# Kernel optimization log

Measured on AMD Instinct MI355X. Metric: run time of the kernel, lower is better.

## Reference

```python
import jax, jax.numpy as jnp
import numpy as np

N = 50000
E = 800000
EPS = 1e-5


def setup_inputs() -> dict:
    key = jax.random.key(0)
    ks = jax.random.split(key, 12)

    def w(k, fi, fo):
        return jax.random.normal(k, (fi, fo), dtype=jnp.float32) * (1.0 / np.sqrt(fi))

    return {
        "x": jax.random.normal(ks[0], (N, 128), dtype=jnp.float32),
        "edge_index": jax.random.randint(ks[1], (2, E), 0, N, dtype=jnp.int32),
        "W1": w(ks[2], 128, 256), "b1": jnp.zeros((256,), jnp.float32),
        "g1": jnp.ones((256,), jnp.float32), "be1": jnp.zeros((256,), jnp.float32),
        "W2": w(ks[3], 256, 128), "b2": jnp.zeros((128,), jnp.float32),
        "g2": jnp.ones((128,), jnp.float32), "be2": jnp.zeros((128,), jnp.float32),
        "W3": w(ks[4], 128, 64), "b3": jnp.zeros((64,), jnp.float32),
        "g3": jnp.ones((64,), jnp.float32), "be3": jnp.zeros((64,), jnp.float32),
        "W4": w(ks[5], 64, 40), "b4": jnp.zeros((40,), jnp.float32),
        "a": jnp.array(0.25, dtype=jnp.float32),  # PReLU single shared weight
    }


def _gcn_norm(edge_index, n):
    # PyG GCNConv default: add self-loops, symmetric normalization.
    loop = jnp.arange(n, dtype=edge_index.dtype)
    s = jnp.concatenate([edge_index[0], loop])  # [E+N] source nodes
    d = jnp.concatenate([edge_index[1], loop])  # [E+N] dest nodes
    deg = jax.ops.segment_sum(jnp.ones_like(s, dtype=jnp.float32), d, num_segments=n)
    dinv = jax.lax.rsqrt(jnp.maximum(deg, 1.0))  # deg >= 1 due to self-loops
    norm = dinv[s] * dinv[d]                     # [E+N]
    return s, d, norm


def _gcn_conv(x, W, b, s, d, norm, n):
    xw = x @ W                                   # [N, F_out] dense transform
    msg = xw[s] * norm[:, None]                  # gather + edge scaling
    return jax.ops.segment_sum(msg, d, num_segments=n) + b  # scatter-add


def _bn(x, g, b):
    # BatchNorm over nodes (training statistics, biased variance)
    m = jnp.mean(x, axis=0)
    v = jnp.var(x, axis=0)
    return (x - m) * jax.lax.rsqrt(v + EPS) * g + b


def _prelu(x, a):
    return jnp.where(x >= 0, x, a * x)


def reference(x, edge_index, W1, b1, g1, be1, W2, b2, g2, be2,
              W3, b3, g3, be3, W4, b4, a):
    n = x.shape[0]
    s, d, norm = _gcn_norm(edge_index, n)
    h = _prelu(_bn(_gcn_conv(x, W1, b1, s, d, norm, n), g1, be1), a)
    h = _prelu(_bn(_gcn_conv(h, W2, b2, s, d, norm, n), g2, be2), a)
    h = _prelu(_bn(_gcn_conv(h, W3, b3, s, d, norm, n), g3, be3), a)
    h = _gcn_conv(h, W4, b4, s, d, norm, n)
    return jax.nn.log_softmax(h, axis=1)
```

## Files before the change

### kernel.cpp

```cpp
#include <hip/hip_runtime.h>
#include <cstdint>
#include <cmath>

typedef _Float16 half_t;
typedef _Float16 h2 __attribute__((ext_vector_type(2)));
typedef _Float16 h8 __attribute__((ext_vector_type(8)));
typedef float f4 __attribute__((ext_vector_type(4)));


__global__ __launch_bounds__(256) void csr_hist_kernel(const int* __restrict__ ei_dst,
                                                       int* __restrict__ hcnt,
                                                       int E, int B, int NB, int chunk) {
    __shared__ int hist[256];
    int t = threadIdx.x;
    hist[t] = 0;
    __syncthreads();
    int base = blockIdx.x * chunk;
    int lim = min(base + chunk, E);
    for (int e = base + t; e < lim; e += 256) {
        int dst = ei_dst[e];
        atomicAdd(&hist[dst >> 8], 1);
    }
    __syncthreads();
    if (t < B) hcnt[t * NB + blockIdx.x] = hist[t];
}

__global__ __launch_bounds__(256) void csr_bscan_kernel(int* __restrict__ hcnt,
                                                        int* __restrict__ btot, int NB) {
    __shared__ int sh[256];
    int b = blockIdx.x, t = threadIdx.x;
    int v = (t < NB) ? hcnt[b * NB + t] : 0;
    sh[t] = v;
    __syncthreads();
    for (int off = 1; off < 256; off <<= 1) {
        int u = (t >= off) ? sh[t - off] : 0;
        __syncthreads();
        sh[t] += u;
        __syncthreads();
    }
    if (t < NB) hcnt[b * NB + t] = sh[t] - v;
    if (t == 255) btot[b] = sh[255];
}

__global__ __launch_bounds__(256) void csr_ebase_kernel(const int* __restrict__ btot,
                                                        int* __restrict__ edge_base,
                                                        int* __restrict__ row_ptr,
                                                        int B, int E, int n) {
    __shared__ int sh[256];
    int t = threadIdx.x;
    int v = (t < B) ? btot[t] : 0;
    sh[t] = v;
    __syncthreads();
    for (int off = 1; off < 256; off <<= 1) {
        int u = (t >= off) ? sh[t - off] : 0;
        __syncthreads();
        sh[t] += u;
        __syncthreads();
    }
    if (t < B) edge_base[t] = sh[t] - v;
    if (t == 0) {
        edge_base[B] = E;
        row_ptr[n] = E;
    }
}

__global__ __launch_bounds__(256) void csr_part_kernel(const int* __restrict__ ei,
                                                       const int* __restrict__ hcnt,
                                                       const int* __restrict__ edge_base,
                                                       unsigned int* __restrict__ ebuf,
                                                       int E, int B, int NB, int chunk) {
    __shared__ int lcur[256];
    int t = threadIdx.x;
    if (t < B) lcur[t] = edge_base[t] + hcnt[t * NB + blockIdx.x];
    __syncthreads();
    int base = blockIdx.x * chunk;
    int lim = min(base + chunk, E);
    for (int e = base + t; e < lim; e += 256) {
        int src = ei[e];
        int dst = ei[E + e];
        int b = dst >> 8;
        int pos = atomicAdd(&lcur[b], 1);
        ebuf[pos] = ((unsigned int)(dst & 255) << 16) | (unsigned int)src;
    }
}

__global__ __launch_bounds__(256) void csr_fill_kernel(const unsigned int* __restrict__ ebuf,
                                                       const int* __restrict__ edge_base,
                                                       int* __restrict__ row_ptr,
                                                       float* __restrict__ dinv,
                                                       unsigned short* __restrict__ colidx,
                                                       int n) {
    __shared__ int cnt[256];
    __shared__ int sc[256];
    __shared__ int cur[256];
    int b = blockIdx.x;
    int t = threadIdx.x;
    int seg_beg = edge_base[b];
    int seg_end = edge_base[b + 1];
    cnt[t] = 0;
    __syncthreads();
    for (int e = seg_beg + t; e < seg_end; e += 256)
        atomicAdd(&cnt[ebuf[e] >> 16], 1);
    __syncthreads();
    sc[t] = cnt[t];
    __syncthreads();
    for (int off = 1; off < 256; off <<= 1) {
        int u = (t >= off) ? sc[t - off] : 0;
        __syncthreads();
        sc[t] += u;
        __syncthreads();
    }
    int excl = seg_beg + sc[t] - cnt[t];
    int node = (b << 8) + t;
    if (node < n) {
        row_ptr[node] = excl;
        dinv[node] = rsqrtf((float)cnt[t] + 1.0f);
    }
    cur[t] = excl;
    __syncthreads();
    for (int e = seg_beg + t; e < seg_end; e += 256) {
        unsigned int p = ebuf[e];
        int pos = atomicAdd(&cur[p >> 16], 1);
        colidx[pos] = (unsigned short)(p & 0xffff);
    }
}


__global__ void f2h_kernel(const float* __restrict__ x, half_t* __restrict__ xh, int total4) {
    int i = blockIdx.x * blockDim.x + threadIdx.x;
    if (i < total4) {
        float4 v = *(const float4*)&x[i * 4];
        half_t* p = xh + (size_t)i * 4;
        p[0] = (half_t)v.x; p[1] = (half_t)v.y; p[2] = (half_t)v.z; p[3] = (half_t)v.w;
    }
}

__global__ void wt_kernel(const float* __restrict__ W, half_t* __restrict__ Wt,
                          int K, int Nc, int Ncp) {
    int idx = blockIdx.x * blockDim.x + threadIdx.x;
    if (idx >= Ncp * K) return;
    int n = idx / K, k = idx - n * K;
    Wt[idx] = (n < Nc) ? (half_t)W[(size_t)k * Nc + n] : (half_t)0.f;
}


__global__ __launch_bounds__(256) void aggh128_kernel(const half_t* __restrict__ in,
                                                      half_t* __restrict__ out,
                                                      const int* __restrict__ row_ptr,
                                                      const unsigned short* __restrict__ colidx,
                                                      const float* __restrict__ dinv, int n) {
    int node = blockIdx.x * 4 + (threadIdx.x >> 6);
    if (node >= n) return;
    int c = threadIdx.x & 63;
    float dv = dinv[node];
    h2 self = *(const h2*)(in + (size_t)node * 128 + 2 * c);
    float acc0 = dv * (float)self[0], acc1 = dv * (float)self[1];
    int beg = row_ptr[node], end = row_ptr[node + 1];
    int k = beg;
    for (; k + 3 < end; k += 4) {
        int s0 = colidx[k], s1 = colidx[k + 1], s2 = colidx[k + 2], s3 = colidx[k + 3];
        float d0 = dinv[s0], d1 = dinv[s1], d2 = dinv[s2], d3 = dinv[s3];
        h2 v0 = *(const h2*)(in + (size_t)s0 * 128 + 2 * c);
        h2 v1 = *(const h2*)(in + (size_t)s1 * 128 + 2 * c);
        h2 v2 = *(const h2*)(in + (size_t)s2 * 128 + 2 * c);
        h2 v3 = *(const h2*)(in + (size_t)s3 * 128 + 2 * c);
        acc0 = fmaf(d0, (float)v0[0], acc0); acc1 = fmaf(d0, (float)v0[1], acc1);
        acc0 = fmaf(d1, (float)v1[0], acc0); acc1 = fmaf(d1, (float)v1[1], acc1);
        acc0 = fmaf(d2, (float)v2[0], acc0); acc1 = fmaf(d2, (float)v2[1], acc1);
        acc0 = fmaf(d3, (float)v3[0], acc0); acc1 = fmaf(d3, (float)v3[1], acc1);
    }
    for (; k < end; ++k) {
        int s = colidx[k];
        float ds = dinv[s];
        h2 v = *(const h2*)(in + (size_t)s * 128 + 2 * c);
        acc0 = fmaf(ds, (float)v[0], acc0);
        acc1 = fmaf(ds, (float)v[1], acc1);
    }
    h2 r;
    r[0] = (half_t)(dv * acc0);
    r[1] = (half_t)(dv * acc1);
    *(h2*)(out + (size_t)node * 128 + 2 * c) = r;
}

__global__ __launch_bounds__(256) void aggh64_kernel(const half_t* __restrict__ in,
                                                     half_t* __restrict__ out,
                                                     const int* __restrict__ row_ptr,
                                                     const unsigned short* __restrict__ colidx,
                                                     const float* __restrict__ dinv, int n) {
    int node = blockIdx.x * 4 + (threadIdx.x >> 6);
    if (node >= n) return;
    int c = threadIdx.x & 63;
    float dv = dinv[node];
    float acc = dv * (float)in[(size_t)node * 64 + c];
    int beg = row_ptr[node], end = row_ptr[node + 1];
    int k = beg;
    for (; k + 3 < end; k += 4) {
        int s0 = colidx[k], s1 = colidx[k + 1], s2 = colidx[k + 2], s3 = colidx[k + 3];
        float d0 = dinv[s0], d1 = dinv[s1], d2 = dinv[s2], d3 = dinv[s3];
        float v0 = (float)in[(size_t)s0 * 64 + c];
        float v1 = (float)in[(size_t)s1 * 64 + c];
        float v2 = (float)in[(size_t)s2 * 64 + c];
        float v3 = (float)in[(size_t)s3 * 64 + c];
        acc = fmaf(d0, v0, acc);
        acc = fmaf(d1, v1, acc);
        acc = fmaf(d2, v2, acc);
        acc = fmaf(d3, v3, acc);
    }
    for (; k < end; ++k) {
        int s = colidx[k];
        acc = fmaf(dinv[s], (float)in[(size_t)s * 64 + c], acc);
    }
    out[(size_t)node * 64 + c] = (half_t)(dv * acc);
}

__global__ __launch_bounds__(256) void aggh_softmax_kernel(const half_t* __restrict__ in,
                                                           float* __restrict__ out,
                                                           const int* __restrict__ row_ptr,
                                                           const unsigned short* __restrict__ colidx,
                                                           const float* __restrict__ dinv,
                                                           const float* __restrict__ b4, int n) {
    int node = blockIdx.x * 4 + (threadIdx.x >> 6);
    if (node >= n) return;
    int c = threadIdx.x & 63;
    float dv = dinv[node];
    float acc = 0.f;
    if (c < 40) acc = dv * (float)in[(size_t)node * 40 + c];
    int beg = row_ptr[node], end = row_ptr[node + 1];
    int k = beg;
    for (; k + 3 < end; k += 4) {
        int s0 = colidx[k], s1 = colidx[k + 1], s2 = colidx[k + 2], s3 = colidx[k + 3];
        float d0 = dinv[s0], d1 = dinv[s1], d2 = dinv[s2], d3 = dinv[s3];
        if (c < 40) {
            float v0 = (float)in[(size_t)s0 * 40 + c];
            float v1 = (float)in[(size_t)s1 * 40 + c];
            float v2 = (float)in[(size_t)s2 * 40 + c];
            float v3 = (float)in[(size_t)s3 * 40 + c];
            acc = fmaf(d0, v0, acc);
            acc = fmaf(d1, v1, acc);
            acc = fmaf(d2, v2, acc);
            acc = fmaf(d3, v3, acc);
        }
    }
    for (; k < end; ++k) {
        int s = colidx[k];
        if (c < 40) acc = fmaf(dinv[s], (float)in[(size_t)s * 40 + c], acc);
    }
    float z = (c < 40) ? (dv * acc + b4[c]) : -INFINITY;
    float m = z;
#pragma unroll
    for (int off = 32; off > 0; off >>= 1) m = fmaxf(m, __shfl_xor(m, off, 64));
    float e = (c < 40) ? expf(z - m) : 0.f;
    float s = e;
#pragma unroll
    for (int off = 32; off > 0; off >>= 1) s += __shfl_xor(s, off, 64);
    if (c < 40) out[(size_t)node * 40 + c] = z - m - logf(s);
}


template <int K, int NT, bool FUSE>
__global__ __launch_bounds__(256) void mgemm_kernel(const half_t* __restrict__ A,
                                                    const half_t* __restrict__ Wt,
                                                    const float* __restrict__ AB,
                                                    const float* __restrict__ pa,
                                                    half_t* __restrict__ C,
                                                    int M, int Nc, int nTiles) {
    constexpr int NR = NT * 16;
    constexpr int CH = K / 8;
    constexpr int LOG_CH = (CH == 8) ? 3 : (CH == 16 ? 4 : 5);
    __shared__ half_t wlds[NR * K];

    for (int idx = threadIdx.x; idx < NR * CH; idx += 256) {
        int row = idx >> LOG_CH;
        int c = idx & (CH - 1);
        *(h8*)(wlds + ((size_t)c * NR + row) * 8) = *(const h8*)(Wt + (size_t)idx * 8);
    }
    int wave = threadIdx.x >> 6;
    int lane = threadIdx.x & 63;
    int l16 = lane & 15, kgrp = lane >> 4;
    float alpha = FUSE ? pa[0] : 0.f;
    __syncthreads();

    for (int tile = blockIdx.x; tile < nTiles; tile += gridDim.x) {
        int r0 = tile * 64 + wave * 16;
        int arow = r0 + l16;
        bool rowok = (arow < M);
        const half_t* Ap = A + (size_t)arow * K + kgrp * 8;
        h8 af[K / 32];
#pragma unroll
        for (int kk = 0; kk < K / 32; ++kk) {
            h8 v;
            if (rowok) {
                v = *(const h8*)(Ap + kk * 32);
            } else {
#pragma unroll
                for (int j = 0; j < 8; ++j) v[j] = (half_t)0.f;
            }
            if (FUSE) {
                int kb = kk * 32 + kgrp * 8;
#pragma unroll
                for (int j = 0; j < 8; ++j) {
                    float u = (float)v[j] * AB[kb + j] + AB[256 + kb + j];
                    u = (u >= 0.f) ? u : alpha * u;
                    v[j] = (half_t)u;
                }
            }
            af[kk] = v;
        }

        for (int nt = 0; nt < NT; ++nt) {
            f4 acc = {0.f, 0.f, 0.f, 0.f};
#pragma unroll
            for (int kk = 0; kk < K / 32; ++kk) {
                h8 bf = *(const h8*)(wlds + ((size_t)(kk * 4 + kgrp) * NR + nt * 16 + l16) * 8);
                acc = __builtin_amdgcn_mfma_f32_16x16x32_f16(af[kk], bf, acc, 0, 0, 0);
            }
            int col = nt * 16 + l16;
            if (col < Nc) {
#pragma unroll
                for (int j = 0; j < 4; ++j) {
                    int row = r0 + kgrp * 4 + j;
                    if (row < M) C[(size_t)row * Nc + col] = (half_t)acc[j];
                }
            }
        }
    }
}


template <int F>
__global__ __launch_bounds__(256) void stats2_kernel(const half_t* __restrict__ z,
                                                     float* __restrict__ sums, int n) {
    constexpr int CB = F / 8;
    constexpr int RG = 256 / CB;
    __shared__ float red[256][16];
    int t = threadIdx.x;
    int cb = t % CB;
    int rg = t / CB;
    float sm[8], sq[8];
#pragma unroll
    for (int j = 0; j < 8; ++j) { sm[j] = 0.f; sq[j] = 0.f; }
    for (int r = blockIdx.x * RG + rg; r < n; r += gridDim.x * RG) {
        h8 v = *(const h8*)(z + (size_t)r * F + cb * 8);
#pragma unroll
        for (int j = 0; j < 8; ++j) {
            float f = (float)v[j];
            sm[j] += f;
            sq[j] = fmaf(f, f, sq[j]);
        }
    }
#pragma unroll
    for (int j = 0; j < 8; ++j) { red[t][j] = sm[j]; red[t][8 + j] = sq[j]; }
    __syncthreads();
    for (int o = t; o < 2 * F; o += 256) {
        int c = o % F, kind = o / F;
        int cbo = c >> 3, ci = (c & 7) + kind * 8;
        float v = 0.f;
#pragma unroll
        for (int g = 0; g < RG; ++g) v += red[g * CB + cbo][ci];
        atomicAdd(&sums[kind * 256 + c], v);
    }
}

__global__ void bnfin_kernel(const float* __restrict__ sums, const float* __restrict__ g,
                             const float* __restrict__ be, float* __restrict__ AB, int n, int F) {
    int c = threadIdx.x;
    if (c >= F) return;
    float mean = sums[c] / (float)n;
    float var = sums[256 + c] / (float)n - mean * mean;
    float rstd = rsqrtf(var + 1e-5f);
    float sc = g[c] * rstd;
    AB[c] = sc;
    AB[256 + c] = be[c] - mean * sc;
}


extern "C" void kernel_launch(void* const* d_in, const int* in_sizes, int n_in,
                              void* d_out, int out_size, void* d_ws, size_t ws_size,
                              hipStream_t stream) {
    const float* x   = (const float*)d_in[0];
    const int*   ei  = (const int*)d_in[1];
    const float* W1  = (const float*)d_in[2];
    const float* g1  = (const float*)d_in[4];
    const float* be1 = (const float*)d_in[5];
    const float* W2  = (const float*)d_in[6];
    const float* g2  = (const float*)d_in[8];
    const float* be2 = (const float*)d_in[9];
    const float* W3  = (const float*)d_in[10];
    const float* g3  = (const float*)d_in[12];
    const float* be3 = (const float*)d_in[13];
    const float* W4  = (const float*)d_in[14];
    const float* b4  = (const float*)d_in[15];
    const float* pa  = (const float*)d_in[16];

    int N = in_sizes[0] / 128;
    int E = in_sizes[1] / 2;
    int B = (N + 255) >> 8;
    int chunk = (((E + 255) / 256) + 255) & ~255;
    int NB = (E + chunk - 1) / chunk;

    char* ws = (char*)d_ws;
    size_t off = 0;
    auto carve = [&](size_t bytes) -> char* {
        char* p = ws + off;
        off += (bytes + 255) & ~(size_t)255;
        return p;
    };
    float*          dinv      = (float*)carve((size_t)N * 4);
    int*            row_ptr   = (int*)carve((size_t)(N + 1) * 4);
    int*            hcnt      = (int*)carve((size_t)B * NB * 4);
    int*            btot      = (int*)carve((size_t)B * 4);
    int*            edge_base = (int*)carve((size_t)(B + 1) * 4);
    unsigned int*   ebuf      = (unsigned int*)carve((size_t)E * 4);
    unsigned short* colidx    = (unsigned short*)carve((size_t)E * 2);
    float*          stats     = (float*)carve(512 * 4);
    float*          bnAB      = (float*)carve(512 * 4);
    half_t* W1t = (half_t*)carve((size_t)256 * 128 * 2);
    half_t* W2t = (half_t*)carve((size_t)128 * 256 * 2);
    half_t* W3t = (half_t*)carve((size_t)64 * 128 * 2);
    half_t* W4t = (half_t*)carve((size_t)48 * 64 * 2);
    half_t* hA  = (half_t*)carve((size_t)N * 256 * 2);
    half_t* hB  = (half_t*)carve((size_t)N * 128 * 2);
    half_t* hC  = (half_t*)carve((size_t)N * 128 * 2);
    half_t* hD1 = (half_t*)carve((size_t)N * 64 * 2);
    half_t* hD2 = (half_t*)carve((size_t)N * 64 * 2);
    half_t* hE  = (half_t*)carve((size_t)N * 40 * 2);
    (void)n_in; (void)out_size; (void)ws_size;

    csr_hist_kernel<<<NB, 256, 0, stream>>>(ei + E, hcnt, E, B, NB, chunk);
    csr_bscan_kernel<<<B, 256, 0, stream>>>(hcnt, btot, NB);
    csr_ebase_kernel<<<1, 256, 0, stream>>>(btot, edge_base, row_ptr, B, E, N);
    csr_part_kernel<<<NB, 256, 0, stream>>>(ei, hcnt, edge_base, ebuf, E, B, NB, chunk);
    csr_fill_kernel<<<B, 256, 0, stream>>>(ebuf, edge_base, row_ptr, dinv, colidx, N);

    wt_kernel<<<(256 * 128 + 255) / 256, 256, 0, stream>>>(W1, W1t, 128, 256, 256);
    wt_kernel<<<(128 * 256 + 255) / 256, 256, 0, stream>>>(W2, W2t, 256, 128, 128);
    wt_kernel<<<(64 * 128 + 255) / 256, 256, 0, stream>>>(W3, W3t, 128, 64, 64);
    wt_kernel<<<(48 * 64 + 255) / 256, 256, 0, stream>>>(W4, W4t, 64, 40, 48);

    int nTiles = (N + 63) / 64;
    int gb = nTiles < 512 ? nTiles : 512;
    int ab = (N + 3) / 4;

    f2h_kernel<<<(N * 128 / 4 + 255) / 256, 256, 0, stream>>>(x, hB, N * 128 / 4);
    aggh128_kernel<<<ab, 256, 0, stream>>>(hB, hC, row_ptr, colidx, dinv, N);
    mgemm_kernel<128, 16, false><<<gb, 256, 0, stream>>>(hC, W1t, nullptr, nullptr, hA,
                                                         N, 256, nTiles);
    hipMemsetAsync(stats, 0, 512 * 4, stream);
    stats2_kernel<256><<<512, 256, 0, stream>>>(hA, stats, N);
    bnfin_kernel<<<1, 256, 0, stream>>>(stats, g1, be1, bnAB, N, 256);

    mgemm_kernel<256, 8, true><<<gb, 256, 0, stream>>>(hA, W2t, bnAB, pa, hB, N, 128, nTiles);
    aggh128_kernel<<<ab, 256, 0, stream>>>(hB, hC, row_ptr, colidx, dinv, N);
    hipMemsetAsync(stats, 0, 512 * 4, stream);
    stats2_kernel<128><<<512, 256, 0, stream>>>(hC, stats, N);
    bnfin_kernel<<<1, 256, 0, stream>>>(stats, g2, be2, bnAB, N, 128);

    mgemm_kernel<128, 4, true><<<gb, 256, 0, stream>>>(hC, W3t, bnAB, pa, hD1, N, 64, nTiles);
    aggh64_kernel<<<ab, 256, 0, stream>>>(hD1, hD2, row_ptr, colidx, dinv, N);
    hipMemsetAsync(stats, 0, 512 * 4, stream);
    stats2_kernel<64><<<512, 256, 0, stream>>>(hD2, stats, N);
    bnfin_kernel<<<1, 256, 0, stream>>>(stats, g3, be3, bnAB, N, 64);

    mgemm_kernel<64, 3, true><<<gb, 256, 0, stream>>>(hD2, W4t, bnAB, pa, hE, N, 40, nTiles);
    aggh_softmax_kernel<<<ab, 256, 0, stream>>>(hE, (float*)d_out, row_ptr, colidx, dinv, b4, N);
}
```

Measured before the change: 317.0 us.

## Merge weight transposes, batch memsets, unroll gathers by 8, pad final layer to 64

The four weight-transpose launches become one kernel, and the three per-layer stats memsets become a single memset over a buffer three times larger, so fewer launches are issued. The neighbour-aggregation loops now unroll by 8 with a masked tail, which puts more gathers in flight. colidx is padded and zeroed so the unmasked index reads past the end stay in bounds. The last layer's output is padded from 40 to 64 columns so the final aggregation plus log-softmax can read h2 pairs with 32 lanes. The padding adds extra GEMM and gather work, and the loop predicate wastes lanes on low-degree nodes.

```diff
diff --git a/kernel.cpp b/kernel.cpp
--- a/kernel.cpp
+++ b/kernel.cpp
@@ -135,12 +135,31 @@
     }
 }
 
-__global__ void wt_kernel(const float* __restrict__ W, half_t* __restrict__ Wt,
-                          int K, int Nc, int Ncp) {
+__global__ __launch_bounds__(256) void wtall_kernel(const float* __restrict__ W1,
+                                                    const float* __restrict__ W2,
+                                                    const float* __restrict__ W3,
+                                                    const float* __restrict__ W4,
+                                                    half_t* __restrict__ W1t,
+                                                    half_t* __restrict__ W2t,
+                                                    half_t* __restrict__ W3t,
+                                                    half_t* __restrict__ W4t) {
     int idx = blockIdx.x * blockDim.x + threadIdx.x;
-    if (idx >= Ncp * K) return;
-    int n = idx / K, k = idx - n * K;
-    Wt[idx] = (n < Nc) ? (half_t)W[(size_t)k * Nc + n] : (half_t)0.f;
+    if (idx < 32768) {
+        int n = idx >> 7, k = idx & 127;
+        W1t[idx] = (half_t)W1[k * 256 + n];
+    } else if (idx < 65536) {
+        int r = idx - 32768;
+        int n = r >> 8, k = r & 255;
+        W2t[r] = (half_t)W2[k * 128 + n];
+    } else if (idx < 73728) {
+        int r = idx - 65536;
+        int n = r >> 7, k = r & 127;
+        W3t[r] = (half_t)W3[k * 64 + n];
+    } else if (idx < 77824) {
+        int r = idx - 73728;
+        int n = r >> 6, k = r & 63;
+        W4t[r] = (n < 40) ? (half_t)W4[k * 40 + n] : (half_t)0.f;
+    }
 }
 
 
@@ -156,25 +175,19 @@
     h2 self = *(const h2*)(in + (size_t)node * 128 + 2 * c);
     float acc0 = dv * (float)self[0], acc1 = dv * (float)self[1];
     int beg = row_ptr[node], end = row_ptr[node + 1];
-    int k = beg;
-    for (; k + 3 < end; k += 4) {
-        int s0 = colidx[k], s1 = colidx[k + 1], s2 = colidx[k + 2], s3 = colidx[k + 3];
-        float d0 = dinv[s0], d1 = dinv[s1], d2 = dinv[s2], d3 = dinv[s3];
-        h2 v0 = *(const h2*)(in + (size_t)s0 * 128 + 2 * c);
-        h2 v1 = *(const h2*)(in + (size_t)s1 * 128 + 2 * c);
-        h2 v2 = *(const h2*)(in + (size_t)s2 * 128 + 2 * c);
-        h2 v3 = *(const h2*)(in + (size_t)s3 * 128 + 2 * c);
-        acc0 = fmaf(d0, (float)v0[0], acc0); acc1 = fmaf(d0, (float)v0[1], acc1);
-        acc0 = fmaf(d1, (float)v1[0], acc0); acc1 = fmaf(d1, (float)v1[1], acc1);
-        acc0 = fmaf(d2, (float)v2[0], acc0); acc1 = fmaf(d2, (float)v2[1], acc1);
-        acc0 = fmaf(d3, (float)v3[0], acc0); acc1 = fmaf(d3, (float)v3[1], acc1);
-    }
-    for (; k < end; ++k) {
-        int s = colidx[k];
-        float ds = dinv[s];
-        h2 v = *(const h2*)(in + (size_t)s * 128 + 2 * c);
-        acc0 = fmaf(ds, (float)v[0], acc0);
-        acc1 = fmaf(ds, (float)v[1], acc1);
+    for (int k = beg; k < end; k += 8) {
+        int idx[8]; float w[8]; h2 v[8];
+#pragma unroll
+        for (int j = 0; j < 8; ++j) idx[j] = colidx[k + j];
+#pragma unroll
+        for (int j = 0; j < 8; ++j) w[j] = (k + j < end) ? dinv[idx[j]] : 0.f;
+#pragma unroll
+        for (int j = 0; j < 8; ++j) v[j] = *(const h2*)(in + (size_t)idx[j] * 128 + 2 * c);
+#pragma unroll
+        for (int j = 0; j < 8; ++j) {
+            acc0 = fmaf(w[j], (float)v[j][0], acc0);
+            acc1 = fmaf(w[j], (float)v[j][1], acc1);
+        }
     }
     h2 r;
     r[0] = (half_t)(dv * acc0);
@@ -193,67 +206,63 @@
     float dv = dinv[node];
     float acc = dv * (float)in[(size_t)node * 64 + c];
     int beg = row_ptr[node], end = row_ptr[node + 1];
-    int k = beg;
-    for (; k + 3 < end; k += 4) {
-        int s0 = colidx[k], s1 = colidx[k + 1], s2 = colidx[k + 2], s3 = colidx[k + 3];
-        float d0 = dinv[s0], d1 = dinv[s1], d2 = dinv[s2], d3 = dinv[s3];
-        float v0 = (float)in[(size_t)s0 * 64 + c];
-        float v1 = (float)in[(size_t)s1 * 64 + c];
-        float v2 = (float)in[(size_t)s2 * 64 + c];
-        float v3 = (float)in[(size_t)s3 * 64 + c];
-        acc = fmaf(d0, v0, acc);
-        acc = fmaf(d1, v1, acc);
-        acc = fmaf(d2, v2, acc);
-        acc = fmaf(d3, v3, acc);
-    }
-    for (; k < end; ++k) {
-        int s = colidx[k];
-        acc = fmaf(dinv[s], (float)in[(size_t)s * 64 + c], acc);
+    for (int k = beg; k < end; k += 8) {
+        int idx[8]; float w[8]; float v[8];
+#pragma unroll
+        for (int j = 0; j < 8; ++j) idx[j] = colidx[k + j];
+#pragma unroll
+        for (int j = 0; j < 8; ++j) w[j] = (k + j < end) ? dinv[idx[j]] : 0.f;
+#pragma unroll
+        for (int j = 0; j < 8; ++j) v[j] = (float)in[(size_t)idx[j] * 64 + c];
+#pragma unroll
+        for (int j = 0; j < 8; ++j) acc = fmaf(w[j], v[j], acc);
     }
     out[(size_t)node * 64 + c] = (half_t)(dv * acc);
 }
 
-__global__ __launch_bounds__(256) void aggh_softmax_kernel(const half_t* __restrict__ in,
-                                                           float* __restrict__ out,
-                                                           const int* __restrict__ row_ptr,
-                                                           const unsigned short* __restrict__ colidx,
-                                                           const float* __restrict__ dinv,
-                                                           const float* __restrict__ b4, int n) {
+__global__ __launch_bounds__(256) void aggsm64_kernel(const half_t* __restrict__ in,
+                                                      float* __restrict__ out,
+                                                      const int* __restrict__ row_ptr,
+                                                      const unsigned short* __restrict__ colidx,
+                                                      const float* __restrict__ dinv,
+                                                      const float* __restrict__ b4, int n) {
     int node = blockIdx.x * 4 + (threadIdx.x >> 6);
     if (node >= n) return;
-    int c = threadIdx.x & 63;
+    int c = threadIdx.x & 31;
     float dv = dinv[node];
-    float acc = 0.f;
-    if (c < 40) acc = dv * (float)in[(size_t)node * 40 + c];
+    h2 self = *(const h2*)(in + (size_t)node * 64 + 2 * c);
+    float acc0 = dv * (float)self[0], acc1 = dv * (float)self[1];
     int beg = row_ptr[node], end = row_ptr[node + 1];
-    int k = beg;
-    for (; k + 3 < end; k += 4) {
-        int s0 = colidx[k], s1 = colidx[k + 1], s2 = colidx[k + 2], s3 = colidx[k + 3];
-        float d0 = dinv[s0], d1 = dinv[s1], d2 = dinv[s2], d3 = dinv[s3];
-        if (c < 40) {
-            float v0 = (float)in[(size_t)s0 * 40 + c];
-            float v1 = (float)in[(size_t)s1 * 40 + c];
-            float v2 = (float)in[(size_t)s2 * 40 + c];
-            float v3 = (float)in[(size_t)s3 * 40 + c];
-            acc = fmaf(d0, v0, acc);
-            acc = fmaf(d1, v1, acc);
-            acc = fmaf(d2, v2, acc);
-            acc = fmaf(d3, v3, acc);
+    for (int k = beg; k < end; k += 8) {
+        int idx[8]; float w[8]; h2 v[8];
+#pragma unroll
+        for (int j = 0; j < 8; ++j) idx[j] = colidx[k + j];
+#pragma unroll
+        for (int j = 0; j < 8; ++j) w[j] = (k + j < end) ? dinv[idx[j]] : 0.f;
+#pragma unroll
+        for (int j = 0; j < 8; ++j) v[j] = *(const h2*)(in + (size_t)idx[j] * 64 + 2 * c);
+#pragma unroll
+        for (int j = 0; j < 8; ++j) {
+            acc0 = fmaf(w[j], (float)v[j][0], acc0);
+            acc1 = fmaf(w[j], (float)v[j][1], acc1);
         }
     }
-    for (; k < end; ++k) {
-        int s = colidx[k];
-        if (c < 40) acc = fmaf(dinv[s], (float)in[(size_t)s * 40 + c], acc);
-    }
-    float z = (c < 40) ? (dv * acc + b4[c]) : -INFINITY;
-    float m = z;
-#pragma unroll
-    for (int off = 32; off > 0; off >>= 1) m = fmaxf(m, __shfl_xor(m, off, 64));
-    float e = (c < 40) ? expf(z - m) : 0.f;
-    float s = e;
-#pragma unroll
-    for (int off = 32; off > 0; off >>= 1) s += __shfl_xor(s, off, 64);
-    if (c < 40) out[(size_t)node * 40 + c] = z - m - logf(s);
+    int col0 = 2 * c, col1 = 2 * c + 1;
+    float z0 = (col0 < 40) ? (dv * acc0 + b4[col0]) : -INFINITY;
+    float z1 = (col1 < 40) ? (dv * acc1 + b4[col1]) : -INFINITY;
+    float m = fmaxf(z0, z1);
+#pragma unroll
+    for (int off = 16; off > 0; off >>= 1) m = fmaxf(m, __shfl_xor(m, off, 64));
+    float e0 = (col0 < 40) ? expf(z0 - m) : 0.f;
+    float e1 = (col1 < 40) ? expf(z1 - m) : 0.f;
+    float s = e0 + e1;
+#pragma unroll
+    for (int off = 16; off > 0; off >>= 1) s += __shfl_xor(s, off, 64);
+    float ls = logf(s);
+    if (c < 20) {
+        float2 r = make_float2(z0 - m - ls, z1 - m - ls);
+        *(float2*)(out + (size_t)node * 40 + 2 * c) = r;
+    }
 }
 
 
@@ -411,20 +420,23 @@
     int*            btot      = (int*)carve((size_t)B * 4);
     int*            edge_base = (int*)carve((size_t)(B + 1) * 4);
     unsigned int*   ebuf      = (unsigned int*)carve((size_t)E * 4);
-    unsigned short* colidx    = (unsigned short*)carve((size_t)E * 2);
-    float*          stats     = (float*)carve(512 * 4);
+    unsigned short* colidx    = (unsigned short*)carve((size_t)(E + 16) * 2);
+    float*          stats     = (float*)carve(3 * 512 * 4);
     float*          bnAB      = (float*)carve(512 * 4);
     half_t* W1t = (half_t*)carve((size_t)256 * 128 * 2);
     half_t* W2t = (half_t*)carve((size_t)128 * 256 * 2);
     half_t* W3t = (half_t*)carve((size_t)64 * 128 * 2);
-    half_t* W4t = (half_t*)carve((size_t)48 * 64 * 2);
+    half_t* W4t = (half_t*)carve((size_t)64 * 64 * 2);
     half_t* hA  = (half_t*)carve((size_t)N * 256 * 2);
     half_t* hB  = (half_t*)carve((size_t)N * 128 * 2);
     half_t* hC  = (half_t*)carve((size_t)N * 128 * 2);
     half_t* hD1 = (half_t*)carve((size_t)N * 64 * 2);
     half_t* hD2 = (half_t*)carve((size_t)N * 64 * 2);
-    half_t* hE  = (half_t*)carve((size_t)N * 40 * 2);
+    half_t* hE  = (half_t*)carve((size_t)N * 64 * 2);
     (void)n_in; (void)out_size; (void)ws_size;
+
+    hipMemsetAsync(colidx + E, 0, 32, stream);
+    hipMemsetAsync(stats, 0, 3 * 512 * 4, stream);
 
     csr_hist_kernel<<<NB, 256, 0, stream>>>(ei + E, hcnt, E, B, NB, chunk);
     csr_bscan_kernel<<<B, 256, 0, stream>>>(hcnt, btot, NB);
@@ -432,10 +444,7 @@
     csr_part_kernel<<<NB, 256, 0, stream>>>(ei, hcnt, edge_base, ebuf, E, B, NB, chunk);
     csr_fill_kernel<<<B, 256, 0, stream>>>(ebuf, edge_base, row_ptr, dinv, colidx, N);
 
-    wt_kernel<<<(256 * 128 + 255) / 256, 256, 0, stream>>>(W1, W1t, 128, 256, 256);
-    wt_kernel<<<(128 * 256 + 255) / 256, 256, 0, stream>>>(W2, W2t, 256, 128, 128);
-    wt_kernel<<<(64 * 128 + 255) / 256, 256, 0, stream>>>(W3, W3t, 128, 64, 64);
-    wt_kernel<<<(48 * 64 + 255) / 256, 256, 0, stream>>>(W4, W4t, 64, 40, 48);
+    wtall_kernel<<<(77824 + 255) / 256, 256, 0, stream>>>(W1, W2, W3, W4, W1t, W2t, W3t, W4t);
 
     int nTiles = (N + 63) / 64;
     int gb = nTiles < 512 ? nTiles : 512;
@@ -445,22 +454,19 @@
     aggh128_kernel<<<ab, 256, 0, stream>>>(hB, hC, row_ptr, colidx, dinv, N);
     mgemm_kernel<128, 16, false><<<gb, 256, 0, stream>>>(hC, W1t, nullptr, nullptr, hA,
                                                          N, 256, nTiles);
-    hipMemsetAsync(stats, 0, 512 * 4, stream);
     stats2_kernel<256><<<512, 256, 0, stream>>>(hA, stats, N);
     bnfin_kernel<<<1, 256, 0, stream>>>(stats, g1, be1, bnAB, N, 256);
 
     mgemm_kernel<256, 8, true><<<gb, 256, 0, stream>>>(hA, W2t, bnAB, pa, hB, N, 128, nTiles);
     aggh128_kernel<<<ab, 256, 0, stream>>>(hB, hC, row_ptr, colidx, dinv, N);
-    hipMemsetAsync(stats, 0, 512 * 4, stream);
-    stats2_kernel<128><<<512, 256, 0, stream>>>(hC, stats, N);
-    bnfin_kernel<<<1, 256, 0, stream>>>(stats, g2, be2, bnAB, N, 128);
+    stats2_kernel<128><<<512, 256, 0, stream>>>(hC, stats + 512, N);
+    bnfin_kernel<<<1, 256, 0, stream>>>(stats + 512, g2, be2, bnAB, N, 128);
 
     mgemm_kernel<128, 4, true><<<gb, 256, 0, stream>>>(hC, W3t, bnAB, pa, hD1, N, 64, nTiles);
     aggh64_kernel<<<ab, 256, 0, stream>>>(hD1, hD2, row_ptr, colidx, dinv, N);
-    hipMemsetAsync(stats, 0, 512 * 4, stream);
-    stats2_kernel<64><<<512, 256, 0, stream>>>(hD2, stats, N);
-    bnfin_kernel<<<1, 256, 0, stream>>>(stats, g3, be3, bnAB, N, 64);
-
-    mgemm_kernel<64, 3, true><<<gb, 256, 0, stream>>>(hD2, W4t, bnAB, pa, hE, N, 40, nTiles);
-    aggh_softmax_kernel<<<ab, 256, 0, stream>>>(hE, (float*)d_out, row_ptr, colidx, dinv, b4, N);
-}
+    stats2_kernel<64><<<512, 256, 0, stream>>>(hD2, stats + 1024, N);
+    bnfin_kernel<<<1, 256, 0, stream>>>(stats + 1024, g3, be3, bnAB, N, 64);
+
+    mgemm_kernel<64, 4, true><<<gb, 256, 0, stream>>>(hD2, W4t, bnAB, pa, hE, N, 64, nTiles);
+    aggsm64_kernel<<<ab, 256, 0, stream>>>(hE, (float*)d_out, row_ptr, colidx, dinv, b4, N);
+}
```

New measurement: 298.2 us. -5.9%, faster.
